# Kernel optimization log

Measured on AMD Instinct MI355X. Metric: run time of the kernel, lower is better.

The kernel has to match this reference:

```python
import jax, jax.numpy as jnp
import numpy as np
import math

B, N, D_IN, D, D_OUT, H = 4, 2048, 128, 128, 256, 4  # D = dim_hidden//2


def _lin(key, din, dout):
    k1, k2 = jax.random.split(key)
    s = 1.0 / math.sqrt(din)
    W = jax.random.uniform(k1, (din, dout), jnp.float32, -s, s)
    b = jax.random.uniform(k2, (dout,), jnp.float32, -s, s)
    return W, b


def setup_inputs() -> dict:
    key = jax.random.key(0)
    ks = jax.random.split(key, 20)
    inp = {"X": jax.random.normal(ks[0], (B, N, D_IN), jnp.float32)}
    # mab dims: (dim_Q, dim_K) -> dim_V=D for each of the 3 MABs
    mab_dims = [(D_IN, D_IN), (D, D), (D, D)]
    ki = 1
    for i, (dq, dk) in enumerate(mab_dims):
        inp[f"m{i}_Wq"], inp[f"m{i}_bq"] = _lin(ks[ki], dq, D); ki += 1
        inp[f"m{i}_Wk"], inp[f"m{i}_bk"] = _lin(ks[ki], dk, D); ki += 1
        inp[f"m{i}_Wv"], inp[f"m{i}_bv"] = _lin(ks[ki], dk, D); ki += 1
        inp[f"m{i}_Wo"], inp[f"m{i}_bo"] = _lin(ks[ki], D, D); ki += 1
    a = math.sqrt(6.0 / (D + 1))  # xavier_uniform for S [1,1,D]
    inp["S"] = jax.random.uniform(ks[ki], (1, 1, D), jnp.float32, -a, a); ki += 1
    inp["pW"], inp["pb"] = _lin(ks[ki], D, D_OUT)
    return inp


def _mab(Q, K, Wq, bq, Wk, bk, Wv, bv, Wo, bo):
    # Linear projections
    Qp = Q @ Wq + bq                       # [B, Nq, D]
    Kp = K @ Wk + bk                       # [B, Nk, D]
    Vp = K @ Wv + bv                       # [B, Nk, D]
    b, nq, dV = Qp.shape
    dh = dV // H
    # torch split(dim_split,2)+cat(0) == head-split on last dim
    Qh = Qp.reshape(b, nq, H, dh)
    Kh = Kp.reshape(b, -1, H, dh)
    Vh = Vp.reshape(b, -1, H, dh)
    # sigmoid attention (no softmax normalizer)
    A = jax.nn.sigmoid(jnp.einsum('bnhd,bmhd->bhnm', Qh, Kh) / jnp.sqrt(jnp.float32(dV)))
    O = Qh + jnp.einsum('bhnm,bmhd->bnhd', A, Vh)
    O = O.reshape(b, nq, dV)
    # residual ReLU-FFN (no LayerNorm since ln=False)
    return O + jax.nn.relu(O @ Wo + bo)


def reference(X,
              m0_Wq, m0_bq, m0_Wk, m0_bk, m0_Wv, m0_bv, m0_Wo, m0_bo,
              m1_Wq, m1_bq, m1_Wk, m1_bk, m1_Wv, m1_bv, m1_Wo, m1_bo,
              m2_Wq, m2_bq, m2_Wk, m2_bk, m2_Wv, m2_bv, m2_Wo, m2_bo,
              S, pW, pb):
    # SAB layer 0: self-attention, dim_in -> D
    Xh = _mab(X, X, m0_Wq, m0_bq, m0_Wk, m0_bk, m0_Wv, m0_bv, m0_Wo, m0_bo)
    # SAB layer 1: D -> D
    Xh = _mab(Xh, Xh, m1_Wq, m1_bq, m1_Wk, m1_bk, m1_Wv, m1_bv, m1_Wo, m1_bo)
    # PMA pooling: seed queries attend over the set
    Sb = jnp.broadcast_to(S, (Xh.shape[0], S.shape[1], S.shape[2]))
    P = _mab(Sb, Xh, m2_Wq, m2_bq, m2_Wk, m2_bk, m2_Wv, m2_bv, m2_Wo, m2_bo)
    # final projection D -> dim_hidden
    return P @ pW + pb  # [B, num_seeds, D_OUT]
```

## Files before the change

kernel.cpp:

```cpp
#include <hip/hip_runtime.h>
#include <hip/hip_bf16.h>

typedef __hip_bfloat16 HB;
typedef __attribute__((ext_vector_type(8))) short short8;
typedef __attribute__((ext_vector_type(4))) short short4v;
typedef __attribute__((ext_vector_type(4))) float f32x4;
typedef __attribute__((ext_vector_type(2))) unsigned int uint2v;
typedef __attribute__((ext_vector_type(4))) unsigned int uint4v;

constexpr int Bn = 4, Nn = 2048, Dm = 128, Hh = 4;
constexpr int MN = Bn * Nn;
constexpr size_t SZ = (size_t)MN * Dm;

static __device__ __forceinline__ short f2bs(float x) {
    __hip_bfloat16 h = __float2bfloat16(x);
    return __builtin_bit_cast(short, h);
}
static __device__ __forceinline__ unsigned int pk2(float lo, float hi) {
    unsigned int a = __builtin_bit_cast(unsigned int, lo) + 0x8000u;
    unsigned int b = __builtin_bit_cast(unsigned int, hi) + 0x8000u;
    return (a >> 16) | (b & 0xFFFF0000u);
}

__global__ void k_wprep(const float* __restrict__ Wa, const float* __restrict__ Wb,
                        const float* __restrict__ Wc, const float* __restrict__ Wd,
                        const float* __restrict__ We, const float* __restrict__ Wf,
                        const float* __restrict__ Wg, const float* __restrict__ Wh,
                        const float* __restrict__ Wi, const float* __restrict__ Wj,
                        HB* __restrict__ WtAll) {
    const float* src;
    switch (blockIdx.x) {
        case 0: src = Wa; break; case 1: src = Wb; break;
        case 2: src = Wc; break; case 3: src = Wd; break;
        case 4: src = We; break; case 5: src = Wf; break;
        case 6: src = Wg; break; case 7: src = Wh; break;
        case 8: src = Wi; break; default: src = Wj; break;
    }
    HB* dst = WtAll + (size_t)blockIdx.x * 16384;
    #pragma unroll
    for (int it = 0; it < 8; ++it) {
        int idx = it * 256 + threadIdx.x;
        int g = idx >> 7, c = idx & 127;
        short8 p;
        #pragma unroll
        for (int j = 0; j < 8; ++j) p[j] = f2bs(src[(size_t)(g * 8 + j) * 128 + c]);
        *(short8*)((short*)dst + (size_t)idx * 8) = p;
    }
}

template<int NW, int RELU, int NEXTRA>
__global__ __launch_bounds__(512) void k_linm(
        const float* __restrict__ A, const float* __restrict__ extra,
        const HB* __restrict__ Wt0, const float* __restrict__ b0,
        const HB* __restrict__ Wt1, const float* __restrict__ b1,
        const HB* __restrict__ Wt2, const float* __restrict__ b2,
        float* __restrict__ C0, float* __restrict__ C1, float* __restrict__ C2) {
    const int tid = threadIdx.x;
    const int w = tid >> 6, lane = tid & 63, l15 = lane & 15, quad = lane >> 4;
    const int row0 = blockIdx.x * 32 + (w >> 2) * 16;
    const int cbase = (w & 3) * 32;

    short8 af[4];
    #pragma unroll
    for (int kc = 0; kc < 4; ++kc) {
        const float* ap = A + (size_t)(row0 + l15) * 128 + kc * 32 + quad * 8;
        float4 x0 = *(const float4*)ap;
        float4 x1 = *(const float4*)(ap + 4);
        if (NEXTRA) {
            const float* ep = extra + (size_t)(row0 + l15) * 128 + kc * 32 + quad * 8;
            float4 e0 = *(const float4*)ep, e1 = *(const float4*)(ep + 4);
            x0.x += e0.x; x0.y += e0.y; x0.z += e0.z; x0.w += e0.w;
            x1.x += e1.x; x1.y += e1.y; x1.z += e1.z; x1.w += e1.w;
        }
        uint4v u;
        u[0] = pk2(x0.x, x0.y); u[1] = pk2(x0.z, x0.w);
        u[2] = pk2(x1.x, x1.y); u[3] = pk2(x1.z, x1.w);
        af[kc] = __builtin_bit_cast(short8, u);
    }

    f32x4 zero = {0.f, 0.f, 0.f, 0.f};
    #pragma unroll
    for (int ct = 0; ct < 2; ++ct) {
        const int col = cbase + ct * 16 + l15;
        #pragma unroll
        for (int s = 0; s < NW; ++s) {
            const HB* Wt = (s == 0) ? Wt0 : (s == 1) ? Wt1 : Wt2;
            const float* bs = (s == 0) ? b0 : (s == 1) ? b1 : b2;
            float* Cs = (s == 0) ? C0 : (s == 1) ? C1 : C2;
            f32x4 acc = zero;
            #pragma unroll
            for (int kc = 0; kc < 4; ++kc) {
                short8 bf = *(const short8*)((const short*)Wt + ((size_t)(kc * 4 + quad) * 128 + col) * 8);
                acc = __builtin_amdgcn_mfma_f32_16x16x32_bf16(af[kc], bf, acc, 0, 0, 0);
            }
            float bb = bs[col];
            #pragma unroll
            for (int r = 0; r < 4; ++r) {
                int row = row0 + quad * 4 + r;
                float v = acc[r] + bb;
                if (RELU) {
                    float st = A[(size_t)row * 128 + col];
                    if (NEXTRA) st += extra[(size_t)row * 128 + col];
                    v = fmaxf(v, 0.f) + st;
                }
                Cs[(size_t)row * 128 + col] = v;
            }
        }
    }
}

__global__ void k_cvt(const float* __restrict__ in, HB* __restrict__ out, int n) {
    int i = (blockIdx.x * 256 + threadIdx.x) * 4;
    if (i + 3 < n) {
        float4 v = *(const float4*)(in + i);
        uint2v p; p[0] = pk2(v.x, v.y); p[1] = pk2(v.z, v.w);
        *(short4v*)((short*)out + i) = __builtin_bit_cast(short4v, p);
    }
}

__global__ void k_vt(const float* __restrict__ Vp, HB* __restrict__ Vt) {
    const int bh = blockIdx.x, b = bh >> 2, h = bh & 3;
    const int n0 = blockIdx.y * 64;
    __shared__ float t[64][33];
    const int tid = threadIdx.x;
    #pragma unroll
    for (int it = 0; it < 2; ++it) {
        int f = it * 256 + tid;
        int r = f >> 3, c4 = f & 7;
        float4 v = *(const float4*)(Vp + (size_t)(b * Nn + n0 + r) * Dm + h * 32 + c4 * 4);
        t[r][c4 * 4 + 0] = v.x; t[r][c4 * 4 + 1] = v.y;
        t[r][c4 * 4 + 2] = v.z; t[r][c4 * 4 + 3] = v.w;
    }
    __syncthreads();
    const int c = tid >> 3, g = tid & 7;
    #pragma unroll
    for (int half = 0; half < 2; ++half) {
        int m = g * 8 + half * 4;
        int slot = (m & ~31) + (((m & 15) >> 2) << 3) + (((m >> 4) & 1) << 2);
        short4v p;
        #pragma unroll
        for (int k = 0; k < 4; ++k) p[k] = f2bs(t[m + k][c]);
        *(short4v*)((short*)Vt + (size_t)(bh * 32 + c) * Nn + n0 + slot) = p;
    }
}

__global__ __launch_bounds__(256) void k_attn3(const float* __restrict__ Qp, const HB* __restrict__ Kbf,
                                               const HB* __restrict__ Vt, float* __restrict__ Opart) {
    const int tid = threadIdx.x;
    const int w = tid >> 6, lane = tid & 63, l15 = lane & 15, quad = lane >> 4;
    const int bh = blockIdx.x >> 6, qg = blockIdx.x & 63;
    const int b = bh >> 2, h = bh & 3;

    __shared__ float ldsacc[4][32][36];

    const float nscale = -0.08838834764831845f;

    short8 aq[2];
    #pragma unroll
    for (int qa = 0; qa < 2; ++qa) {
        const float* qp = Qp + (size_t)(b * Nn + qg * 32 + qa * 16 + l15) * 128 + h * 32 + quad * 8;
        float4 q0 = *(const float4*)qp;
        float4 q1 = *(const float4*)(qp + 4);
        uint4v u;
        u[0] = pk2(q0.x, q0.y); u[1] = pk2(q0.z, q0.w);
        u[2] = pk2(q1.x, q1.y); u[3] = pk2(q1.z, q1.w);
        aq[qa] = __builtin_bit_cast(short8, u);
    }

    f32x4 zero = {0.f, 0.f, 0.f, 0.f};
    f32x4 o[2][2];
    o[0][0] = zero; o[0][1] = zero; o[1][0] = zero; o[1][1] = zero;

    const short* Kb = (const short*)Kbf + (size_t)b * Nn * 128 + h * 32;
    const short* Vb = (const short*)Vt + (size_t)bh * 32 * Nn;

    for (int m0 = w * 512; m0 < w * 512 + 512; m0 += 64) {
        short8 kb[4];
        #pragma unroll
        for (int mc = 0; mc < 4; ++mc)
            kb[mc] = *(const short8*)(Kb + (size_t)(m0 + mc * 16 + l15) * 128 + quad * 8);
        short8 vf[2][2];
        #pragma unroll
        for (int t = 0; t < 2; ++t)
            #pragma unroll
            for (int u = 0; u < 2; ++u)
                vf[t][u] = *(const short8*)(Vb + (size_t)(t * 16 + l15) * Nn + m0 + u * 32 + quad * 8);

        #pragma unroll
        for (int qa = 0; qa < 2; ++qa) {
            f32x4 s[4];
            #pragma unroll
            for (int mc = 0; mc < 4; ++mc)
                s[mc] = __builtin_amdgcn_mfma_f32_16x16x32_bf16(kb[mc], aq[qa], zero, 0, 0, 0);
            #pragma unroll
            for (int u = 0; u < 2; ++u) {
                f32x4 lo = s[2 * u], hi = s[2 * u + 1];
                float p0 = __builtin_amdgcn_rcpf(1.f + __expf(lo[0] * nscale));
                float p1 = __builtin_amdgcn_rcpf(1.f + __expf(lo[1] * nscale));
                float p2 = __builtin_amdgcn_rcpf(1.f + __expf(lo[2] * nscale));
                float p3 = __builtin_amdgcn_rcpf(1.f + __expf(lo[3] * nscale));
                float p4 = __builtin_amdgcn_rcpf(1.f + __expf(hi[0] * nscale));
                float p5 = __builtin_amdgcn_rcpf(1.f + __expf(hi[1] * nscale));
                float p6 = __builtin_amdgcn_rcpf(1.f + __expf(hi[2] * nscale));
                float p7 = __builtin_amdgcn_rcpf(1.f + __expf(hi[3] * nscale));
                uint4v pu;
                pu[0] = pk2(p0, p1); pu[1] = pk2(p2, p3);
                pu[2] = pk2(p4, p5); pu[3] = pk2(p6, p7);
                short8 pf = __builtin_bit_cast(short8, pu);
                #pragma unroll
                for (int t = 0; t < 2; ++t)
                    o[qa][t] = __builtin_amdgcn_mfma_f32_16x16x32_bf16(vf[t][u], pf, o[qa][t], 0, 0, 0);
            }
        }
    }

    #pragma unroll
    for (int qa = 0; qa < 2; ++qa)
        #pragma unroll
        for (int t = 0; t < 2; ++t)
            *(f32x4*)&ldsacc[w][qa * 16 + l15][t * 16 + quad * 4] = o[qa][t];
    __syncthreads();
    const int row = tid >> 3, cc = (tid & 7) * 4;
    f32x4 r0 = *(f32x4*)&ldsacc[0][row][cc];
    f32x4 r1 = *(f32x4*)&ldsacc[1][row][cc];
    f32x4 r2 = *(f32x4*)&ldsacc[2][row][cc];
    f32x4 r3 = *(f32x4*)&ldsacc[3][row][cc];
    f32x4 sum = (r0 + r1) + (r2 + r3);
    *(f32x4*)(Opart + (size_t)(b * Nn + qg * 32 + row) * 128 + h * 32 + cc) = sum;
}

__global__ void k_pma2(const float* __restrict__ S, const float* __restrict__ Wq, const float* __restrict__ bq,
                       const float* __restrict__ Kp, const float* __restrict__ Vp,
                       float* __restrict__ P0part) {
    const int bh = blockIdx.x, b = bh >> 2, h = bh & 3;
    const int ms = blockIdx.y;
    const int tid = threadIdx.x;
    __shared__ float4 qs4[8];
    float* qs = (float*)qs4;
    if (tid < 32) {
        float a = bq[h * 32 + tid];
        for (int k = 0; k < 128; ++k)
            a = fmaf(S[k], Wq[k * Dm + h * 32 + tid], a);
        qs[tid] = a;
    }
    __syncthreads();

    float4 q[8];
    #pragma unroll
    for (int i = 0; i < 8; ++i) q[i] = qs4[i];

    const size_t base = (size_t)b * Nn * Dm + h * 32;
    const float nscale = -0.08838834764831845f;
    const int m = ms * 256 + tid;

    const float4* kp = (const float4*)(Kp + base + (size_t)m * Dm);
    const float4* vp = (const float4*)(Vp + base + (size_t)m * Dm);
    float d0 = 0.f, d1 = 0.f, d2 = 0.f, d3 = 0.f;
    #pragma unroll
    for (int c = 0; c < 8; c += 4) {
        float4 k0 = kp[c+0], k1 = kp[c+1], k2 = kp[c+2], k3 = kp[c+3];
        d0 += q[c+0].x*k0.x + q[c+0].y*k0.y + q[c+0].z*k0.z + q[c+0].w*k0.w;
        d1 += q[c+1].x*k1.x + q[c+1].y*k1.y + q[c+1].z*k1.z + q[c+1].w*k1.w;
        d2 += q[c+2].x*k2.x + q[c+2].y*k2.y + q[c+2].z*k2.z + q[c+2].w*k2.w;
        d3 += q[c+3].x*k3.x + q[c+3].y*k3.y + q[c+3].z*k3.z + q[c+3].w*k3.w;
    }
    float dot = (d0 + d1) + (d2 + d3);
    float a = __builtin_amdgcn_rcpf(1.f + __expf(dot * nscale));
    float4 acc[8];
    #pragma unroll
    for (int c = 0; c < 8; ++c) {
        float4 vv = vp[c];
        acc[c].x = a * vv.x; acc[c].y = a * vv.y; acc[c].z = a * vv.z; acc[c].w = a * vv.w;
    }
    #pragma unroll
    for (int off = 1; off < 64; off <<= 1) {
        #pragma unroll
        for (int c = 0; c < 8; ++c) {
            acc[c].x += __shfl_xor(acc[c].x, off);
            acc[c].y += __shfl_xor(acc[c].y, off);
            acc[c].z += __shfl_xor(acc[c].z, off);
            acc[c].w += __shfl_xor(acc[c].w, off);
        }
    }
    __shared__ float red[4][32];
    const int wave = tid >> 6, lane = tid & 63;
    if (lane == 0) {
        #pragma unroll
        for (int c = 0; c < 8; ++c) {
            red[wave][c*4+0] = acc[c].x; red[wave][c*4+1] = acc[c].y;
            red[wave][c*4+2] = acc[c].z; red[wave][c*4+3] = acc[c].w;
        }
    }
    __syncthreads();
    if (tid < 32) {
        float t = (red[0][tid] + red[1][tid]) + (red[2][tid] + red[3][tid]);
        if (ms == 0) t += qs[tid];
        P0part[ms * 512 + b * 128 + h * 32 + tid] = t;
    }
}

__global__ __launch_bounds__(256) void k_lin_small(
                      const float* __restrict__ A,
                      const float* __restrict__ extra, int nextra, int estride,
                      const float* __restrict__ W0, const float* __restrict__ b0,
                      int M, float* __restrict__ C0) {
    __shared__ float ldsf[16 * 128];
    const int tid = threadIdx.x;

    #pragma unroll
    for (int it = 0; it < 2; ++it) {
        int f = it * 256 + tid;
        int r = f >> 5, c = f & 31;
        float4 v = make_float4(0.f, 0.f, 0.f, 0.f);
        if (r < M) {
            v = ((const float4*)(A + (size_t)r * 128))[c];
            for (int e = 0; e < nextra; ++e) {
                float4 w = ((const float4*)(extra + (size_t)e * estride + (size_t)r * 128))[c];
                v.x += w.x; v.y += w.y; v.z += w.z; v.w += w.w;
            }
        }
        ((float4*)ldsf)[f] = v;
    }
    __syncthreads();

    const int col = tid & 127;
    const int rg  = tid >> 7;
    float acc[2] = {0.f, 0.f};
    #pragma unroll 8
    for (int k = 0; k < 128; ++k) {
        float w = W0[k * 128 + col];
        acc[0] = fmaf(ldsf[rg * 128 + k], w, acc[0]);
        acc[1] = fmaf(ldsf[(rg + 2) * 128 + k], w, acc[1]);
    }
    float bb = b0[col];
    #pragma unroll
    for (int i = 0; i < 2; ++i) {
        int r = rg + 2 * i;
        if (r < M) {
            float v = fmaxf(acc[i] + bb, 0.f) + ldsf[r * 128 + col];
            C0[(size_t)r * 128 + col] = v;
        }
    }
}

__global__ void k_final(const float* __restrict__ P, const float* __restrict__ pW,
                        const float* __restrict__ pb, float* __restrict__ out) {
    const int b = blockIdx.x, c = threadIdx.x;
    __shared__ float ps[128];
    if (c < 128) ps[c] = P[b * Dm + c];
    __syncthreads();
    float a = pb[c];
    #pragma unroll 8
    for (int k = 0; k < 128; ++k)
        a = fmaf(ps[k], pW[k * 256 + c], a);
    out[b * 256 + c] = a;
}

extern "C" void kernel_launch(void* const* d_in, const int* in_sizes, int n_in,
                              void* d_out, int out_size, void* d_ws, size_t ws_size,
                              hipStream_t stream) {
    const float* X = (const float*)d_in[0];
    auto W = [&](int i) { return (const float*)d_in[i]; };
    float* ws = (float*)d_ws;

    float* s0 = ws + 0 * SZ;
    float* s1 = ws + 1 * SZ;
    float* s2 = ws + 2 * SZ;
    float* s3 = ws + 3 * SZ;
    HB*    Kbf = (HB*)(ws + 4 * SZ);
    HB*    Vt  = Kbf + SZ;
    HB*    WtAll = (HB*)(ws + 5 * SZ);
    auto Wt = [&](int idx) { return (const HB*)(WtAll + (size_t)idx * 16384); };
    float* P0part = s3;
    float* Pp     = s3 + 8192;

    const int GLM = MN / 32;
    const int GC = (int)(SZ / 4 / 256);
    dim3 vt_grid(Bn * Hh, Nn / 64);
    const int attn_blocks = Bn * Hh * (Nn / 32);
    dim3 pma_grid(Bn * Hh, 8);
    const float* nul = nullptr;
    const HB* nulh = nullptr;

    k_wprep<<<10, 256, 0, stream>>>(W(1), W(3), W(5), W(7), W(9), W(11), W(13), W(15),
                                    W(19), W(21), WtAll);

    k_linm<3,0,0><<<GLM, 512, 0, stream>>>(X, nul, Wt(0), W(2), Wt(1), W(4), Wt(2), W(6),
                                           s0, s2, s1);
    k_cvt<<<GC, 256, 0, stream>>>(s2, Kbf, (int)SZ);
    k_vt<<<vt_grid, 256, 0, stream>>>(s1, Vt);
    k_attn3<<<attn_blocks, 256, 0, stream>>>(s0, Kbf, Vt, s2);
    k_linm<1,1,1><<<GLM, 512, 0, stream>>>(s0, s2, Wt(3), W(8), nulh, nul, nulh, nul,
                                           s3, nullptr, nullptr);

    k_linm<3,0,0><<<GLM, 512, 0, stream>>>(s3, nul, Wt(4), W(10), Wt(5), W(12), Wt(6), W(14),
                                           s0, s2, s1);
    k_cvt<<<GC, 256, 0, stream>>>(s2, Kbf, (int)SZ);
    k_vt<<<vt_grid, 256, 0, stream>>>(s1, Vt);
    k_attn3<<<attn_blocks, 256, 0, stream>>>(s0, Kbf, Vt, s2);
    k_linm<1,1,1><<<GLM, 512, 0, stream>>>(s0, s2, Wt(7), W(16), nulh, nul, nulh, nul,
                                           s1, nullptr, nullptr);

    k_linm<2,0,0><<<GLM, 512, 0, stream>>>(s1, nul, Wt(8), W(20), Wt(9), W(22), nulh, nul,
                                           s0, s2, nullptr);
    k_pma2<<<pma_grid, 256, 0, stream>>>((const float*)d_in[25], W(17), W(18), s0, s2, P0part);
    k_lin_small<<<1, 256, 0, stream>>>(P0part, P0part + 512, 7, 512, W(23), W(24), Bn, Pp);

    k_final<<<Bn, 256, 0, stream>>>(Pp, (const float*)d_in[26], (const float*)d_in[27], (float*)d_out);
}
```

Measured before the change: 251.6 us.

## Fuse K bf16 conversion and V transpose into QKV projection epilogue

The QKV projection kernel now writes K directly as bf16 and writes V directly in the transposed, slot-permuted bf16 layout that the attention kernel expects. This removes the separate k_cvt and k_vt launches and their fp32 round trips through global memory, twice per forward pass. The bf16 packing now uses a byte-permute builtin, and the attention key loop is unrolled by two. The trade-off is scattered 2-byte stores for K and strided short4 stores for V in the projection epilogue, plus a reshuffle of workspace buffers.

Result: faster. 236.7 us (-5.9%).

```diff
diff --git a/kernel.cpp b/kernel.cpp
--- a/kernel.cpp
+++ b/kernel.cpp
@@ -16,10 +16,17 @@
     __hip_bfloat16 h = __float2bfloat16(x);
     return __builtin_bit_cast(short, h);
 }
+static __device__ __forceinline__ unsigned short f2bh(float x) {
+    return (unsigned short)((__builtin_bit_cast(unsigned int, x) + 0x8000u) >> 16);
+}
 static __device__ __forceinline__ unsigned int pk2(float lo, float hi) {
     unsigned int a = __builtin_bit_cast(unsigned int, lo) + 0x8000u;
     unsigned int b = __builtin_bit_cast(unsigned int, hi) + 0x8000u;
+#if __has_builtin(__builtin_amdgcn_perm)
+    return __builtin_amdgcn_perm(b, a, 0x07060302u);
+#else
     return (a >> 16) | (b & 0xFFFF0000u);
+#endif
 }
 
 __global__ void k_wprep(const float* __restrict__ Wa, const float* __restrict__ Wb,
@@ -48,13 +55,14 @@
     }
 }
 
-template<int NW, int RELU, int NEXTRA>
+template<int NW, int RELU, int NEXTRA, int FUSE>
 __global__ __launch_bounds__(512) void k_linm(
         const float* __restrict__ A, const float* __restrict__ extra,
         const HB* __restrict__ Wt0, const float* __restrict__ b0,
         const HB* __restrict__ Wt1, const float* __restrict__ b1,
         const HB* __restrict__ Wt2, const float* __restrict__ b2,
-        float* __restrict__ C0, float* __restrict__ C1, float* __restrict__ C2) {
+        float* __restrict__ C0, float* __restrict__ C1,
+        HB* __restrict__ Kb, HB* __restrict__ Vt) {
     const int tid = threadIdx.x;
     const int w = tid >> 6, lane = tid & 63, l15 = lane & 15, quad = lane >> 4;
     const int row0 = blockIdx.x * 32 + (w >> 2) * 16;
@@ -86,7 +94,6 @@
         for (int s = 0; s < NW; ++s) {
             const HB* Wt = (s == 0) ? Wt0 : (s == 1) ? Wt1 : Wt2;
             const float* bs = (s == 0) ? b0 : (s == 1) ? b1 : b2;
-            float* Cs = (s == 0) ? C0 : (s == 1) ? C1 : C2;
             f32x4 acc = zero;
             #pragma unroll
             for (int kc = 0; kc < 4; ++kc) {
@@ -94,53 +101,37 @@
                 acc = __builtin_amdgcn_mfma_f32_16x16x32_bf16(af[kc], bf, acc, 0, 0, 0);
             }
             float bb = bs[col];
-            #pragma unroll
-            for (int r = 0; r < 4; ++r) {
-                int row = row0 + quad * 4 + r;
-                float v = acc[r] + bb;
-                if (RELU) {
-                    float st = A[(size_t)row * 128 + col];
-                    if (NEXTRA) st += extra[(size_t)row * 128 + col];
-                    v = fmaxf(v, 0.f) + st;
+            if (s == 0 || !FUSE) {
+                float* Cs = (s == 0) ? C0 : C1;
+                #pragma unroll
+                for (int r = 0; r < 4; ++r) {
+                    int row = row0 + quad * 4 + r;
+                    float v = acc[r] + bb;
+                    if (RELU && s == 0) {
+                        float st = A[(size_t)row * 128 + col];
+                        if (NEXTRA) st += extra[(size_t)row * 128 + col];
+                        v = fmaxf(v, 0.f) + st;
+                    }
+                    Cs[(size_t)row * 128 + col] = v;
                 }
-                Cs[(size_t)row * 128 + col] = v;
+            } else if (s == 1) {
+                #pragma unroll
+                for (int r = 0; r < 4; ++r) {
+                    int row = row0 + quad * 4 + r;
+                    ((unsigned short*)Kb)[(size_t)row * 128 + col] = f2bh(acc[r] + bb);
+                }
+            } else {
+                int b_ = row0 >> 11;
+                int mloc = (row0 + quad * 4) & 2047;
+                int slotb = (mloc & ~31) + (((mloc & 15) >> 2) << 3) + (((mloc >> 4) & 1) << 2);
+                int h_ = col >> 5, dh = col & 31;
+                uint2v pv;
+                pv[0] = pk2(acc[0] + bb, acc[1] + bb);
+                pv[1] = pk2(acc[2] + bb, acc[3] + bb);
+                *(short4v*)((short*)Vt + ((size_t)((b_ * 4 + h_) * 32 + dh)) * 2048 + slotb)
+                    = __builtin_bit_cast(short4v, pv);
             }
         }
-    }
-}
-
-__global__ void k_cvt(const float* __restrict__ in, HB* __restrict__ out, int n) {
-    int i = (blockIdx.x * 256 + threadIdx.x) * 4;
-    if (i + 3 < n) {
-        float4 v = *(const float4*)(in + i);
-        uint2v p; p[0] = pk2(v.x, v.y); p[1] = pk2(v.z, v.w);
-        *(short4v*)((short*)out + i) = __builtin_bit_cast(short4v, p);
-    }
-}
-
-__global__ void k_vt(const float* __restrict__ Vp, HB* __restrict__ Vt) {
-    const int bh = blockIdx.x, b = bh >> 2, h = bh & 3;
-    const int n0 = blockIdx.y * 64;
-    __shared__ float t[64][33];
-    const int tid = threadIdx.x;
-    #pragma unroll
-    for (int it = 0; it < 2; ++it) {
-        int f = it * 256 + tid;
-        int r = f >> 3, c4 = f & 7;
-        float4 v = *(const float4*)(Vp + (size_t)(b * Nn + n0 + r) * Dm + h * 32 + c4 * 4);
-        t[r][c4 * 4 + 0] = v.x; t[r][c4 * 4 + 1] = v.y;
-        t[r][c4 * 4 + 2] = v.z; t[r][c4 * 4 + 3] = v.w;
-    }
-    __syncthreads();
-    const int c = tid >> 3, g = tid & 7;
-    #pragma unroll
-    for (int half = 0; half < 2; ++half) {
-        int m = g * 8 + half * 4;
-        int slot = (m & ~31) + (((m & 15) >> 2) << 3) + (((m >> 4) & 1) << 2);
-        short4v p;
-        #pragma unroll
-        for (int k = 0; k < 4; ++k) p[k] = f2bs(t[m + k][c]);
-        *(short4v*)((short*)Vt + (size_t)(bh * 32 + c) * Nn + n0 + slot) = p;
     }
 }
 
@@ -174,6 +165,7 @@
     const short* Kb = (const short*)Kbf + (size_t)b * Nn * 128 + h * 32;
     const short* Vb = (const short*)Vt + (size_t)bh * 32 * Nn;
 
+    #pragma unroll 2
     for (int m0 = w * 512; m0 < w * 512 + 512; m0 += 64) {
         short8 kb[4];
         #pragma unroll
@@ -371,38 +363,33 @@
     HB*    Vt  = Kbf + SZ;
     HB*    WtAll = (HB*)(ws + 5 * SZ);
     auto Wt = [&](int idx) { return (const HB*)(WtAll + (size_t)idx * 16384); };
-    float* P0part = s3;
-    float* Pp     = s3 + 8192;
+    float* P0part = s1;
+    float* Pp     = s1 + 8192;
 
     const int GLM = MN / 32;
-    const int GC = (int)(SZ / 4 / 256);
-    dim3 vt_grid(Bn * Hh, Nn / 64);
     const int attn_blocks = Bn * Hh * (Nn / 32);
     dim3 pma_grid(Bn * Hh, 8);
     const float* nul = nullptr;
     const HB* nulh = nullptr;
+    HB* nulhm = nullptr;
 
     k_wprep<<<10, 256, 0, stream>>>(W(1), W(3), W(5), W(7), W(9), W(11), W(13), W(15),
                                     W(19), W(21), WtAll);
 
-    k_linm<3,0,0><<<GLM, 512, 0, stream>>>(X, nul, Wt(0), W(2), Wt(1), W(4), Wt(2), W(6),
-                                           s0, s2, s1);
-    k_cvt<<<GC, 256, 0, stream>>>(s2, Kbf, (int)SZ);
-    k_vt<<<vt_grid, 256, 0, stream>>>(s1, Vt);
+    k_linm<3,0,0,1><<<GLM, 512, 0, stream>>>(X, nul, Wt(0), W(2), Wt(1), W(4), Wt(2), W(6),
+                                             s0, nullptr, Kbf, Vt);
     k_attn3<<<attn_blocks, 256, 0, stream>>>(s0, Kbf, Vt, s2);
-    k_linm<1,1,1><<<GLM, 512, 0, stream>>>(s0, s2, Wt(3), W(8), nulh, nul, nulh, nul,
-                                           s3, nullptr, nullptr);
-
-    k_linm<3,0,0><<<GLM, 512, 0, stream>>>(s3, nul, Wt(4), W(10), Wt(5), W(12), Wt(6), W(14),
-                                           s0, s2, s1);
-    k_cvt<<<GC, 256, 0, stream>>>(s2, Kbf, (int)SZ);
-    k_vt<<<vt_grid, 256, 0, stream>>>(s1, Vt);
+    k_linm<1,1,1,0><<<GLM, 512, 0, stream>>>(s0, s2, Wt(3), W(8), nulh, nul, nulh, nul,
+                                             s1, nullptr, nulhm, nulhm);
+
+    k_linm<3,0,0,1><<<GLM, 512, 0, stream>>>(s1, nul, Wt(4), W(10), Wt(5), W(12), Wt(6), W(14),
+                                             s0, nullptr, Kbf, Vt);
     k_attn3<<<attn_blocks, 256, 0, stream>>>(s0, Kbf, Vt, s2);
-    k_linm<1,1,1><<<GLM, 512, 0, stream>>>(s0, s2, Wt(7), W(16), nulh, nul, nulh, nul,
-                                           s1, nullptr, nullptr);
-
-    k_linm<2,0,0><<<GLM, 512, 0, stream>>>(s1, nul, Wt(8), W(20), Wt(9), W(22), nulh, nul,
-                                           s0, s2, nullptr);
+    k_linm<1,1,1,0><<<GLM, 512, 0, stream>>>(s0, s2, Wt(7), W(16), nulh, nul, nulh, nul,
+                                             s3, nullptr, nulhm, nulhm);
+
+    k_linm<2,0,0,0><<<GLM, 512, 0, stream>>>(s3, nul, Wt(8), W(20), Wt(9), W(22), nulh, nul,
+                                             s0, s2, nulhm, nulhm);
     k_pma2<<<pma_grid, 256, 0, stream>>>((const float*)d_in[25], W(17), W(18), s0, s2, P0part);
     k_lin_small<<<1, 256, 0, stream>>>(P0part, P0part + 512, 7, 512, W(23), W(24), Bn, Pp);
 
```
